# Performance work log

Measured on AMD Instinct MI355X. Metric: run time of the kernel, lower is better.

The kernel has to match this reference:

```python
import jax, jax.numpy as jnp
import numpy as np

B, S, D, H = 4, 2048, 1024, 16
DH = D // H  # per-head dim = 64


def setup_inputs() -> dict:
    key = jax.random.key(0)
    ks = jax.random.split(key, 7)
    s_in = 1.0 / np.sqrt(D)
    return {
        "x": jax.random.normal(ks[0], (B, S, D), dtype=jnp.float32),
        "Wq": jax.random.normal(ks[1], (H, D, DH), dtype=jnp.float32) * s_in,
        "bq": jnp.zeros((H, DH), dtype=jnp.float32),
        "Wk": jax.random.normal(ks[2], (H, D, DH), dtype=jnp.float32) * s_in,
        "bk": jnp.zeros((H, DH), dtype=jnp.float32),
        "Wv": jax.random.normal(ks[3], (H, D, DH), dtype=jnp.float32) * s_in,
        "bv": jnp.zeros((H, DH), dtype=jnp.float32),
    }


def reference(x, Wq, bq, Wk, bk, Wv, bv):
    # Batched form of the per-head Python loop: all heads in one einsum.
    q = jnp.einsum("bsd,hde->bhse", x, Wq) + bq[None, :, None, :]
    k = jnp.einsum("bsd,hde->bhse", x, Wk) + bk[None, :, None, :]
    v = jnp.einsum("bsd,hde->bhse", x, Wv) + bv[None, :, None, :]
    scale = 1.0 / jnp.sqrt(jnp.asarray(DH, dtype=q.dtype))
    scores = jnp.einsum("bhse,bhte->bhst", q, k) * scale  # [B,H,S,S]
    attn = jax.nn.softmax(scores, axis=-1)
    out = jnp.einsum("bhst,bhte->bhse", attn, v)  # [B,H,S,DH]
    # concat heads along last dim (head order preserved, as torch.cat)
    return out.transpose(0, 2, 1, 3).reshape(B, S, H * DH)
```

## Files before the change

kernel.cpp:

```cpp
#include <hip/hip_runtime.h>
#include <cstdint>
#include <cstddef>

#define B_   4
#define S_   2048
#define D_   1024
#define H_   16
#define DH_  64

typedef __attribute__((ext_vector_type(8))) short short8;
typedef __attribute__((ext_vector_type(4))) float f32x4;

static __device__ __forceinline__ unsigned short f2b(float f){
    unsigned int u = __float_as_uint(f);
    return (unsigned short)((u + 0x7FFFu + ((u >> 16) & 1u)) >> 16);
}

__global__ __launch_bounds__(256)
void cvt_x_kernel(const float* __restrict__ x, unsigned short* __restrict__ xb){
    size_t i0 = ((size_t)blockIdx.x * 256 + threadIdx.x) * 8;
    float4 a = *(const float4*)(x + i0);
    float4 b = *(const float4*)(x + i0 + 4);
    union { unsigned short u[8]; uint4 v; } r;
    r.u[0]=f2b(a.x); r.u[1]=f2b(a.y); r.u[2]=f2b(a.z); r.u[3]=f2b(a.w);
    r.u[4]=f2b(b.x); r.u[5]=f2b(b.y); r.u[6]=f2b(b.z); r.u[7]=f2b(b.w);
    *(uint4*)(xb + i0) = r.v;
}

__global__ __launch_bounds__(256)
void cvt_w_kernel(const float* __restrict__ Wq, const float* __restrict__ Wk,
                  const float* __restrict__ Wv, unsigned short* __restrict__ wt){
    int id = blockIdx.x * 256 + threadIdx.x;
    int e4 = (id & 15) * 4;
    int k  = (id >> 4) & 1023;
    int h  = (id >> 14) & 15;
    int t_ = id >> 18;
    const float* W = (t_ == 0) ? Wq : ((t_ == 1) ? Wk : Wv);
    float4 w = *(const float4*)(W + (((size_t)h * D_ + k) * DH_ + e4));
    unsigned short* dst = wt + (((size_t)t_ * H_ + h) * DH_ + e4) * D_ + k;
    dst[0]            = f2b(w.x);
    dst[(size_t)D_]   = f2b(w.y);
    dst[(size_t)2*D_] = f2b(w.z);
    dst[(size_t)3*D_] = f2b(w.w);
}

__global__ __launch_bounds__(256)
void qkv_proj_mfma(const unsigned short* __restrict__ xb,
                   const unsigned short* __restrict__ wtg,
                   const float* __restrict__ bq, const float* __restrict__ bk,
                   const float* __restrict__ bv,
                   unsigned short* __restrict__ qb,
                   unsigned short* __restrict__ kb,
                   unsigned short* __restrict__ vt)
{
    const int mb  = blockIdx.x;
    const int h   = blockIdx.y;
    const int t   = threadIdx.x;
    const int w   = t >> 6;
    const int l   = t & 63;
    const int l15 = l & 15;
    const int g   = l >> 4;

    __shared__ unsigned short xs[128][72];
    __shared__ unsigned short ws[192][72];
    __shared__ float bias_s[192];

    if (t < 192){
        int tensor = t >> 6, eloc = t & 63;
        const float* bp = (tensor == 0) ? bq : ((tensor == 1) ? bk : bv);
        bias_s[t] = bp[h * DH_ + eloc];
    }

    f32x4 acc[2][12];
#pragma unroll
    for (int mt = 0; mt < 2; ++mt)
#pragma unroll
        for (int nt = 0; nt < 12; ++nt) acc[mt][nt] = (f32x4){0.f,0.f,0.f,0.f};

    const int m0 = mb * 128;

    for (int k0 = 0; k0 < D_; k0 += 64){
        __syncthreads();
#pragma unroll
        for (int it = 0; it < 4; ++it){
            int c = t + it * 256;
            int row = c >> 3, off = (c & 7) * 8;
            *(short8*)&xs[row][off] =
                *(const short8*)(xb + (size_t)(m0 + row) * D_ + k0 + off);
        }
#pragma unroll
        for (int it = 0; it < 6; ++it){
            int c = t + it * 256;
            int row = c >> 3, off = (c & 7) * 8;
            int tensor = row >> 6, eloc = row & 63;
            *(short8*)&ws[row][off] =
                *(const short8*)(wtg + (((size_t)tensor * H_ + h) * DH_ + eloc) * D_ + k0 + off);
        }
        __syncthreads();

#pragma unroll
        for (int ks = 0; ks < 2; ++ks){
            short8 a0 = *(const short8*)&xs[32*w + l15     ][32*ks + g*8];
            short8 a1 = *(const short8*)&xs[32*w + 16 + l15][32*ks + g*8];
#pragma unroll
            for (int nt = 0; nt < 12; ++nt){
                short8 bb = *(const short8*)&ws[16*nt + l15][32*ks + g*8];
                acc[0][nt] = __builtin_amdgcn_mfma_f32_16x16x32_bf16(a0, bb, acc[0][nt], 0,0,0);
                acc[1][nt] = __builtin_amdgcn_mfma_f32_16x16x32_bf16(a1, bb, acc[1][nt], 0,0,0);
            }
        }
    }

    const int b   = m0 >> 11;
    const int bh  = b * H_ + h;
    const int sb  = (m0 & (S_ - 1)) + 32 * w;
#pragma unroll
    for (int mt = 0; mt < 2; ++mt){
        int s0 = sb + 16 * mt + 4 * g;
#pragma unroll
        for (int nt = 0; nt < 12; ++nt){
            float bias = bias_s[16 * nt + l15];
            if (nt < 4){
                int e = 16 * nt + l15;
                size_t base = ((size_t)bh * S_ + s0) * DH_ + e;
#pragma unroll
                for (int r = 0; r < 4; ++r)
                    qb[base + (size_t)r * DH_] = f2b((acc[mt][nt][r] + bias) * 0.125f);
            } else if (nt < 8){
                int e = 16 * (nt - 4) + l15;
                size_t base = ((size_t)bh * S_ + s0) * DH_ + e;
#pragma unroll
                for (int r = 0; r < 4; ++r)
                    kb[base + (size_t)r * DH_] = f2b(acc[mt][nt][r] + bias);
            } else {
                int e = 16 * (nt - 8) + l15;
                union { unsigned short u[4]; uint2 v; } pk;
#pragma unroll
                for (int r = 0; r < 4; ++r) pk.u[r] = f2b(acc[mt][nt][r] + bias);
                *(uint2*)(vt + ((size_t)bh * DH_ + e) * S_ + s0) = pk.v;
            }
        }
    }
}

__global__ __launch_bounds__(256)
void attn_mfma(const unsigned short* __restrict__ qb,
               const unsigned short* __restrict__ kb,
               const unsigned short* __restrict__ vt,
               float* __restrict__ out)
{
    const int qt  = blockIdx.x;
    const int bh  = blockIdx.y;
    const int b   = bh >> 4, h = bh & 15;
    const int t   = threadIdx.x;
    const int w   = t >> 6;
    const int l   = t & 63;
    const int l15 = l & 15;
    const int g   = l >> 4;

    __shared__ unsigned short Kl [64][72];
    __shared__ unsigned short Vtl[64][72];
    __shared__ unsigned short Pl [4][16][72];

    const size_t bhb = (size_t)bh * S_ * DH_;

    short8 qf[2];
    {
        const int qrow = qt * 64 + 16 * w + l15;
        const unsigned short* qp = qb + bhb + (size_t)qrow * DH_ + g * 8;
        qf[0] = *(const short8*)(qp);
        qf[1] = *(const short8*)(qp + 32);
    }

    f32x4 o[4];
#pragma unroll
    for (int nt = 0; nt < 4; ++nt) o[nt] = (f32x4){0.f,0.f,0.f,0.f};
    float m_r = -1e30f, l_r = 0.f;

    for (int kt = 0; kt < S_ / 64; ++kt){
        __syncthreads();
#pragma unroll
        for (int it = 0; it < 2; ++it){
            int c = t + it * 256;
            int row = c >> 3, off = (c & 7) * 8;
            *(short8*)&Kl[row][off] =
                *(const short8*)(kb + bhb + (size_t)(kt * 64 + row) * DH_ + off);
            *(short8*)&Vtl[row][off] =
                *(const short8*)(vt + bhb + (size_t)row * S_ + kt * 64 + off);
        }
        __syncthreads();

        f32x4 st[4];
#pragma unroll
        for (int mt = 0; mt < 4; ++mt) st[mt] = (f32x4){0.f,0.f,0.f,0.f};
#pragma unroll
        for (int ks = 0; ks < 2; ++ks){
#pragma unroll
            for (int mt = 0; mt < 4; ++mt){
                short8 ak = *(const short8*)&Kl[16*mt + l15][32*ks + g*8];
                st[mt] = __builtin_amdgcn_mfma_f32_16x16x32_bf16(ak, qf[ks], st[mt], 0,0,0);
            }
        }

        float pm = -1e30f;
#pragma unroll
        for (int mt = 0; mt < 4; ++mt)
#pragma unroll
            for (int r = 0; r < 4; ++r) pm = fmaxf(pm, st[mt][r]);
        pm = fmaxf(pm, __shfl_xor(pm, 16));
        pm = fmaxf(pm, __shfl_xor(pm, 32));
        float mnew = fmaxf(m_r, pm);
        float corr = __expf(m_r - mnew);
        float lsum = 0.f;
#pragma unroll
        for (int mt = 0; mt < 4; ++mt)
#pragma unroll
            for (int r = 0; r < 4; ++r){
                float p = __expf(st[mt][r] - mnew);
                st[mt][r] = p;
                lsum += p;
            }
        lsum += __shfl_xor(lsum, 16);
        lsum += __shfl_xor(lsum, 32);
        l_r = l_r * corr + lsum;
        m_r = mnew;

        float cr[4];
#pragma unroll
        for (int r = 0; r < 4; ++r) cr[r] = __shfl(corr, 4 * g + r);
#pragma unroll
        for (int nt = 0; nt < 4; ++nt)
#pragma unroll
            for (int r = 0; r < 4; ++r) o[nt][r] *= cr[r];

#pragma unroll
        for (int mt = 0; mt < 4; ++mt){
            unsigned long long pp =
                  (unsigned long long)f2b(st[mt][0])
                | ((unsigned long long)f2b(st[mt][1]) << 16)
                | ((unsigned long long)f2b(st[mt][2]) << 32)
                | ((unsigned long long)f2b(st[mt][3]) << 48);
            *(unsigned long long*)&Pl[w][l15][16 * mt + 4 * g] = pp;
        }
        __syncthreads();

#pragma unroll
        for (int ks = 0; ks < 2; ++ks){
            short8 ap = *(const short8*)&Pl[w][l15][32*ks + g*8];
#pragma unroll
            for (int nt = 0; nt < 4; ++nt){
                short8 bv2 = *(const short8*)&Vtl[16*nt + l15][32*ks + g*8];
                o[nt] = __builtin_amdgcn_mfma_f32_16x16x32_bf16(ap, bv2, o[nt], 0,0,0);
            }
        }
    }

    float invl[4];
#pragma unroll
    for (int r = 0; r < 4; ++r) invl[r] = 1.f / __shfl(l_r, 4 * g + r);
    const int srow0 = qt * 64 + 16 * w + 4 * g;
#pragma unroll
    for (int nt = 0; nt < 4; ++nt)
#pragma unroll
        for (int r = 0; r < 4; ++r)
            out[((size_t)b * S_ + srow0 + r) * D_ + h * DH_ + 16 * nt + l15] =
                o[nt][r] * invl[r];
}

extern "C" void kernel_launch(void* const* d_in, const int* in_sizes, int n_in,
                              void* d_out, int out_size, void* d_ws, size_t ws_size,
                              hipStream_t stream) {
    const float* x  = (const float*)d_in[0];
    const float* Wq = (const float*)d_in[1];
    const float* bq = (const float*)d_in[2];
    const float* Wk = (const float*)d_in[3];
    const float* bk = (const float*)d_in[4];
    const float* Wv = (const float*)d_in[5];
    const float* bv = (const float*)d_in[6];
    float* out = (float*)d_out;

    char* wsp = (char*)d_ws;
    unsigned short* xb  = (unsigned short*)(wsp);
    unsigned short* wtg = (unsigned short*)(wsp + 16777216);
    unsigned short* qb  = (unsigned short*)(wsp + 23068672);
    unsigned short* kb  = (unsigned short*)(wsp + 39845888);
    unsigned short* vt  = (unsigned short*)(wsp + 56623104);

    cvt_x_kernel<<<4096, 256, 0, stream>>>(x, xb);
    cvt_w_kernel<<<3072, 256, 0, stream>>>(Wq, Wk, Wv, wtg);
    qkv_proj_mfma<<<dim3(64, 16), 256, 0, stream>>>(xb, wtg, bq, bk, bv, qb, kb, vt);
    attn_mfma<<<dim3(32, 64), 256, 0, stream>>>(qb, kb, vt, out);
}
```

Measured before the change: 323.9 us.

## Swizzle LDS tiles, use exp2 softmax with lazy rescale, hardware bf16 packing

Replaces padded LDS arrays with XOR-swizzled layouts in both kernels to avoid bank conflicts. Folds log2(e) into the Q scale so softmax uses the raw v_exp_f32 instruction, and skips the output rescale unless the running max grows by more than a threshold. Uses v_cvt_pk_bf16_f32 for P packing, replaces a workgroup barrier with a wave-local lgkmcnt wait since each wave reads only its own P tile, and adds s_setprio around MFMA sections. The lazy-rescale threshold trades a little exponent headroom for fewer corrections.

```diff
diff --git a/kernel.cpp b/kernel.cpp
--- a/kernel.cpp
+++ b/kernel.cpp
@@ -11,9 +11,21 @@
 typedef __attribute__((ext_vector_type(8))) short short8;
 typedef __attribute__((ext_vector_type(4))) float f32x4;
 
+#define SWZ16(row, ch) ((((row) * 8) + (((ch) ^ ((row) & 7)))) * 8)
+
 static __device__ __forceinline__ unsigned short f2b(float f){
     unsigned int u = __float_as_uint(f);
     return (unsigned short)((u + 0x7FFFu + ((u >> 16) & 1u)) >> 16);
+}
+static __device__ __forceinline__ unsigned int cvtpk(float lo, float hi){
+    unsigned int r;
+    asm("v_cvt_pk_bf16_f32 %0, %1, %2" : "=v"(r) : "v"(lo), "v"(hi));
+    return r;
+}
+static __device__ __forceinline__ float exp2_hw(float x){
+    float r;
+    asm("v_exp_f32 %0, %1" : "=v"(r) : "v"(x));
+    return r;
 }
 
 __global__ __launch_bounds__(256)
@@ -61,8 +73,8 @@
     const int l15 = l & 15;
     const int g   = l >> 4;
 
-    __shared__ unsigned short xs[128][72];
-    __shared__ unsigned short ws[192][72];
+    __shared__ unsigned short xs[128 * 64];
+    __shared__ unsigned short ws[192 * 64];
     __shared__ float bias_s[192];
 
     if (t < 192){
@@ -84,33 +96,36 @@
 #pragma unroll
         for (int it = 0; it < 4; ++it){
             int c = t + it * 256;
-            int row = c >> 3, off = (c & 7) * 8;
-            *(short8*)&xs[row][off] =
-                *(const short8*)(xb + (size_t)(m0 + row) * D_ + k0 + off);
+            int row = c >> 3, ch = c & 7;
+            *(short8*)&xs[SWZ16(row, ch)] =
+                *(const short8*)(xb + (size_t)(m0 + row) * D_ + k0 + ch * 8);
         }
 #pragma unroll
         for (int it = 0; it < 6; ++it){
             int c = t + it * 256;
-            int row = c >> 3, off = (c & 7) * 8;
+            int row = c >> 3, ch = c & 7;
             int tensor = row >> 6, eloc = row & 63;
-            *(short8*)&ws[row][off] =
-                *(const short8*)(wtg + (((size_t)tensor * H_ + h) * DH_ + eloc) * D_ + k0 + off);
+            *(short8*)&ws[SWZ16(row, ch)] =
+                *(const short8*)(wtg + (((size_t)tensor * H_ + h) * DH_ + eloc) * D_ + k0 + ch * 8);
         }
         __syncthreads();
 
+        __builtin_amdgcn_s_setprio(1);
 #pragma unroll
         for (int ks = 0; ks < 2; ++ks){
-            short8 a0 = *(const short8*)&xs[32*w + l15     ][32*ks + g*8];
-            short8 a1 = *(const short8*)&xs[32*w + 16 + l15][32*ks + g*8];
+            short8 a0 = *(const short8*)&xs[SWZ16(32*w + l15,      4*ks + g)];
+            short8 a1 = *(const short8*)&xs[SWZ16(32*w + 16 + l15, 4*ks + g)];
 #pragma unroll
             for (int nt = 0; nt < 12; ++nt){
-                short8 bb = *(const short8*)&ws[16*nt + l15][32*ks + g*8];
+                short8 bb = *(const short8*)&ws[SWZ16(16*nt + l15, 4*ks + g)];
                 acc[0][nt] = __builtin_amdgcn_mfma_f32_16x16x32_bf16(a0, bb, acc[0][nt], 0,0,0);
                 acc[1][nt] = __builtin_amdgcn_mfma_f32_16x16x32_bf16(a1, bb, acc[1][nt], 0,0,0);
             }
         }
-    }
-
+        __builtin_amdgcn_s_setprio(0);
+    }
+
+    const float QSCALE = 0.180336880f;
     const int b   = m0 >> 11;
     const int bh  = b * H_ + h;
     const int sb  = (m0 & (S_ - 1)) + 32 * w;
@@ -125,7 +140,7 @@
                 size_t base = ((size_t)bh * S_ + s0) * DH_ + e;
 #pragma unroll
                 for (int r = 0; r < 4; ++r)
-                    qb[base + (size_t)r * DH_] = f2b((acc[mt][nt][r] + bias) * 0.125f);
+                    qb[base + (size_t)r * DH_] = f2b((acc[mt][nt][r] + bias) * QSCALE);
             } else if (nt < 8){
                 int e = 16 * (nt - 4) + l15;
                 size_t base = ((size_t)bh * S_ + s0) * DH_ + e;
@@ -158,9 +173,10 @@
     const int l15 = l & 15;
     const int g   = l >> 4;
 
-    __shared__ unsigned short Kl [64][72];
-    __shared__ unsigned short Vtl[64][72];
-    __shared__ unsigned short Pl [4][16][72];
+    __shared__ unsigned short Kl [64 * 64];
+    __shared__ unsigned short Vtl[64 * 64];
+    __shared__ unsigned short Pl [4 * 16 * 64];
+    unsigned short* Pw = Pl + w * 16 * 64;
 
     const size_t bhb = (size_t)bh * S_ * DH_;
 
@@ -182,25 +198,27 @@
 #pragma unroll
         for (int it = 0; it < 2; ++it){
             int c = t + it * 256;
-            int row = c >> 3, off = (c & 7) * 8;
-            *(short8*)&Kl[row][off] =
-                *(const short8*)(kb + bhb + (size_t)(kt * 64 + row) * DH_ + off);
-            *(short8*)&Vtl[row][off] =
-                *(const short8*)(vt + bhb + (size_t)row * S_ + kt * 64 + off);
+            int row = c >> 3, ch = c & 7;
+            *(short8*)&Kl[SWZ16(row, ch)] =
+                *(const short8*)(kb + bhb + (size_t)(kt * 64 + row) * DH_ + ch * 8);
+            *(short8*)&Vtl[SWZ16(row, ch)] =
+                *(const short8*)(vt + bhb + (size_t)row * S_ + kt * 64 + ch * 8);
         }
         __syncthreads();
 
         f32x4 st[4];
 #pragma unroll
         for (int mt = 0; mt < 4; ++mt) st[mt] = (f32x4){0.f,0.f,0.f,0.f};
+        __builtin_amdgcn_s_setprio(1);
 #pragma unroll
         for (int ks = 0; ks < 2; ++ks){
 #pragma unroll
             for (int mt = 0; mt < 4; ++mt){
-                short8 ak = *(const short8*)&Kl[16*mt + l15][32*ks + g*8];
+                short8 ak = *(const short8*)&Kl[SWZ16(16*mt + l15, 4*ks + g)];
                 st[mt] = __builtin_amdgcn_mfma_f32_16x16x32_bf16(ak, qf[ks], st[mt], 0,0,0);
             }
         }
+        __builtin_amdgcn_s_setprio(0);
 
         float pm = -1e30f;
 #pragma unroll
@@ -209,50 +227,56 @@
             for (int r = 0; r < 4; ++r) pm = fmaxf(pm, st[mt][r]);
         pm = fmaxf(pm, __shfl_xor(pm, 16));
         pm = fmaxf(pm, __shfl_xor(pm, 32));
-        float mnew = fmaxf(m_r, pm);
-        float corr = __expf(m_r - mnew);
+
+        if (__any(pm > m_r + 8.0f)){
+            float mnew = fmaxf(m_r, pm);
+            float corr = exp2_hw(m_r - mnew);
+            float cr[4];
+#pragma unroll
+            for (int r = 0; r < 4; ++r) cr[r] = __shfl(corr, 4 * g + r);
+#pragma unroll
+            for (int nt = 0; nt < 4; ++nt)
+#pragma unroll
+                for (int r = 0; r < 4; ++r) o[nt][r] *= cr[r];
+            l_r *= corr;
+            m_r = mnew;
+        }
+
         float lsum = 0.f;
 #pragma unroll
         for (int mt = 0; mt < 4; ++mt)
 #pragma unroll
             for (int r = 0; r < 4; ++r){
-                float p = __expf(st[mt][r] - mnew);
+                float p = exp2_hw(st[mt][r] - m_r);
                 st[mt][r] = p;
                 lsum += p;
             }
         lsum += __shfl_xor(lsum, 16);
         lsum += __shfl_xor(lsum, 32);
-        l_r = l_r * corr + lsum;
-        m_r = mnew;
-
-        float cr[4];
-#pragma unroll
-        for (int r = 0; r < 4; ++r) cr[r] = __shfl(corr, 4 * g + r);
-#pragma unroll
-        for (int nt = 0; nt < 4; ++nt)
-#pragma unroll
-            for (int r = 0; r < 4; ++r) o[nt][r] *= cr[r];
+        l_r += lsum;
 
 #pragma unroll
         for (int mt = 0; mt < 4; ++mt){
-            unsigned long long pp =
-                  (unsigned long long)f2b(st[mt][0])
-                | ((unsigned long long)f2b(st[mt][1]) << 16)
-                | ((unsigned long long)f2b(st[mt][2]) << 32)
-                | ((unsigned long long)f2b(st[mt][3]) << 48);
-            *(unsigned long long*)&Pl[w][l15][16 * mt + 4 * g] = pp;
-        }
-        __syncthreads();
-
+            uint2 pp;
+            pp.x = cvtpk(st[mt][0], st[mt][1]);
+            pp.y = cvtpk(st[mt][2], st[mt][3]);
+            int pc = 2 * mt + (g >> 1);
+            *(uint2*)(Pw + (l15 * 8 + (pc ^ (l15 & 7))) * 8 + (g & 1) * 4) = pp;
+        }
+        asm volatile("s_waitcnt lgkmcnt(0)" ::: "memory");
+        __builtin_amdgcn_sched_barrier(0);
+
+        __builtin_amdgcn_s_setprio(1);
 #pragma unroll
         for (int ks = 0; ks < 2; ++ks){
-            short8 ap = *(const short8*)&Pl[w][l15][32*ks + g*8];
+            short8 ap = *(const short8*)&Pw[SWZ16(l15, 4*ks + g)];
 #pragma unroll
             for (int nt = 0; nt < 4; ++nt){
-                short8 bv2 = *(const short8*)&Vtl[16*nt + l15][32*ks + g*8];
+                short8 bv2 = *(const short8*)&Vtl[SWZ16(16*nt + l15, 4*ks + g)];
                 o[nt] = __builtin_amdgcn_mfma_f32_16x16x32_bf16(ap, bv2, o[nt], 0,0,0);
             }
         }
+        __builtin_amdgcn_s_setprio(0);
     }
 
     float invl[4];
```

Result: slower. 351.8 us (+8.6%).
